# Optimization experiments

Measured on AMD Instinct MI355X. Metric: run time of the kernel, lower is better.

The kernel has to match this reference:

```python
import jax, jax.numpy as jnp
import numpy as np

B, T, E, D = 256, 128, 256, 256


def setup_inputs() -> dict:
    key = jax.random.key(0)
    ks = jax.random.split(key, 8)
    x = jax.random.normal(ks[0], (B, T, E), dtype=jnp.float32)
    # torch default Linear init: U(-1/sqrt(fan_in), 1/sqrt(fan_in)) for proj layers;
    # TreeLSTMCell.reset_parameters uses U(-1/sqrt(hidden), 1/sqrt(hidden)).
    se = 1.0 / np.sqrt(E)
    sd = 1.0 / np.sqrt(D)
    Wp = jax.random.uniform(ks[1], (E, D), jnp.float32, -se, se)
    bp = jax.random.uniform(ks[2], (D,), jnp.float32, -se, se)
    Wg = jax.random.uniform(ks[3], (E, D), jnp.float32, -se, se)
    bg = jax.random.uniform(ks[4], (D,), jnp.float32, -se, se)
    Wr = jax.random.uniform(ks[5], (2 * D, 5 * D), jnp.float32, -sd, sd)
    br = jax.random.uniform(ks[6], (5 * D,), jnp.float32, -sd, sd)
    # Valid shift-reduce sequence (right-branching): S, then (S, R) x (T-1) -> length 2T-1.
    pat = np.zeros(2 * T - 1, dtype=np.int32)
    pat[2::2] = 1  # REDUCE at odd stack-growth points
    transitions = jnp.asarray(np.broadcast_to(pat[:, None], (2 * T - 1, B)).copy())
    return {"x": x, "Wp": Wp, "bp": bp, "Wg": Wg, "bg": bg,
            "Wr": Wr, "br": br, "transitions": transitions}


def reference(x, Wp, bp, Wg, bg, Wr, br, transitions):
    Bx, Tx, _ = x.shape
    Dh = Wp.shape[1]
    # leaf transformation: c = Wx+b ; h = sigmoid(gate) * tanh(c)
    c_buf = x @ Wp + bp                                   # [B, T, D]
    h_buf = jax.nn.sigmoid(x @ Wg + bg) * jnp.tanh(c_buf)  # [B, T, D]
    buffers = jnp.concatenate([h_buf, c_buf], axis=-1)    # [B, T, 2D]

    stack0 = jnp.zeros((Bx, Tx, 2 * Dh), x.dtype)
    ptr0 = jnp.zeros((Bx,), jnp.int32)          # stack pointer (next free slot)
    bptr0 = jnp.full((Bx,), Tx - 1, jnp.int32)  # buffer pop index (pops from end)
    bidx = jnp.arange(Bx)

    def step(carry, trans_t):
        stack, ptr, bptr = carry
        is_shift = trans_t == 0
        shift_val = buffers[bidx, bptr]                       # [B, 2D]
        r = stack[bidx, jnp.maximum(ptr - 1, 0)]              # right child (top)
        l = stack[bidx, jnp.maximum(ptr - 2, 0)]              # left child
        h_l, c_l = l[:, :Dh], l[:, Dh:]
        h_r, c_r = r[:, :Dh], r[:, Dh:]
        proj = jnp.concatenate([h_l, h_r], axis=-1) @ Wr + br  # [B, 5D]
        i, f_l, f_r, g, o = jnp.split(proj, 5, axis=-1)
        c = (jax.nn.sigmoid(i) * jnp.tanh(g)
             + jax.nn.sigmoid(f_l) * c_l
             + jax.nn.sigmoid(f_r) * c_r)
        h = jax.nn.sigmoid(o) * jnp.tanh(c)
        red = jnp.concatenate([h, c], axis=-1)                # [B, 2D]
        pos = jnp.where(is_shift, ptr, jnp.maximum(ptr - 2, 0))
        val = jnp.where(is_shift[:, None], shift_val, red)
        stack = stack.at[bidx, pos].set(val)
        ptr = ptr + jnp.where(is_shift, jnp.int32(1), jnp.int32(-1))
        bptr = bptr - is_shift.astype(jnp.int32)
        return (stack, ptr, bptr), None

    (stack, ptr, _), _ = jax.lax.scan(step, (stack0, ptr0, bptr0), transitions)
    final = stack[bidx, jnp.maximum(ptr - 1, 0)][:, :Dh]  # root h states [B, D]
    return final
```

## Files before the change

kernel.cpp:

```cpp
#include <hip/hip_runtime.h>


typedef unsigned int u32;
typedef short s16x8 __attribute__((ext_vector_type(8)));
typedef float f32x4 __attribute__((ext_vector_type(4)));

#define NPAIR 128
#define ZCODE 0x801F

#define MFMA16(a, b, c) __builtin_amdgcn_mfma_f32_16x16x32_bf16((a), (b), (c), 0, 0, 0)

static __device__ __forceinline__ unsigned short f2bf(float x) {
  u32 u = __builtin_bit_cast(u32, x);
  u += 0x7fffu + ((u >> 16) & 1u);
  return (unsigned short)(u >> 16);
}
static __device__ __forceinline__ float bf2f(unsigned short s) {
  u32 u = ((u32)s) << 16;
  return __builtin_bit_cast(float, u);
}
static __device__ __forceinline__ u32 packhl(float x) {
  unsigned short hi = f2bf(x);
  unsigned short lo = f2bf(x - bf2f(hi));
  return ((u32)hi << 16) | (u32)lo;
}
static __device__ __forceinline__ float unpackhl(u32 p) {
  return bf2f((unsigned short)(p >> 16)) + bf2f((unsigned short)(p & 0xffffu));
}
static __device__ __forceinline__ void unpack8(uint4 a, uint4 b, s16x8 &hi, s16x8 &lo) {
  hi[0] = (short)(a.x >> 16); lo[0] = (short)a.x;
  hi[1] = (short)(a.y >> 16); lo[1] = (short)a.y;
  hi[2] = (short)(a.z >> 16); lo[2] = (short)a.z;
  hi[3] = (short)(a.w >> 16); lo[3] = (short)a.w;
  hi[4] = (short)(b.x >> 16); lo[4] = (short)b.x;
  hi[5] = (short)(b.y >> 16); lo[5] = (short)b.y;
  hi[6] = (short)(b.z >> 16); lo[6] = (short)b.z;
  hi[7] = (short)(b.w >> 16); lo[7] = (short)b.w;
}
static __device__ __forceinline__ void split8(const float *w, s16x8 &hi, s16x8 &lo) {
#pragma unroll
  for (int i = 0; i < 8; i++) {
    unsigned short h = f2bf(w[i]);
    hi[i] = (short)h;
    lo[i] = (short)f2bf(w[i] - bf2f(h));
  }
}
static __device__ __forceinline__ float sigm(float x) { return 1.0f / (1.0f + expf(-x)); }

__global__ __launch_bounds__(256) void pack_kernel(
    const float *__restrict__ Wp, const float *__restrict__ Wg,
    const float *__restrict__ Wr, u32 *__restrict__ Wpg_t,
    u32 *__restrict__ Wr_t, u32 *__restrict__ vstkH, float *__restrict__ vstkC) {
  int tid = blockIdx.x * 256 + threadIdx.x;
  if (tid < 512 * 256) {
    int col = tid >> 8, k = tid & 255;
    float v = (col < 256) ? Wp[k * 256 + col] : Wg[k * 256 + (col - 256)];
    Wpg_t[tid] = packhl(v);
  }
  if (tid < 1280 * 512) {
    int col = tid >> 9, k = tid & 511;
    Wr_t[tid] = packhl(Wr[k * 1280 + col]);
  }
  if (tid < 65536) {
    vstkH[31 * 65536 + tid] = 0u;
    vstkC[31 * 65536 + tid] = 0.0f;
  }
}

__global__ __launch_bounds__(256) void plan_kernel(
    const int *__restrict__ trans, int *__restrict__ planL,
    int *__restrict__ planR, int *__restrict__ planW, int *__restrict__ fdesc) {
  int b = threadIdx.x;
  int tag[16], ver[16];
#pragma unroll
  for (int i = 0; i < 16; ++i) { tag[i] = ZCODE; ver[i] = 0; }
  int ptr = 0, bptr = 127;

  auto dostep = [&](int tr, int &l, int &r, int &w) {
    if (tr == 0) {
      int pos = min(ptr, 15);
      tag[pos] = bptr & 127;
      ptr++; bptr--;
    } else {
      int pl = min(max(ptr - 2, 0), 15);
      int pr = min(max(ptr - 1, 0), 15);
      l = tag[pl];
      r = tag[pr];
      ver[pl] ^= 1;
      tag[pl] = 0x8000 | (ver[pl] << 4) | pl;
      w = pl * 2 + ver[pl];
      ptr--;
    }
  };

  for (int f = 0; f < NPAIR; ++f) {
    int l = ZCODE, r = ZCODE, w = -1;
    dostep(trans[(2 * f) * 256 + b], l, r, w);
    if (2 * f + 1 < 255) dostep(trans[(2 * f + 1) * 256 + b], l, r, w);
    planL[f * 256 + b] = l;
    planR[f * 256 + b] = r;
    planW[f * 256 + b] = w;
  }
  fdesc[b] = tag[min(max(ptr - 1, 0), 15)];
}

__global__ __launch_bounds__(64) void front_kernel(
    const float *__restrict__ x, const u32 *__restrict__ Wpg,
    const float *__restrict__ bp, const float *__restrict__ bg,
    u32 *__restrict__ h_buf, float *__restrict__ c_buf) {
  const int lane = threadIdx.x;
  const int rbase = blockIdx.x * 32;
  const int y = blockIdx.y;
  const int rlo = lane & 15;
  const int khi = (lane >> 4) * 8;

  f32x4 z = {0.f, 0.f, 0.f, 0.f};
  f32x4 aP0[8], aP1[8], aG0[8], aG1[8];
#pragma unroll
  for (int i = 0; i < 8; i++) { aP0[i] = z; aP1[i] = z; aG0[i] = z; aG1[i] = z; }

#pragma unroll 2
  for (int kt = 0; kt < 8; ++kt) {
    int k = kt * 32 + khi;
    s16x8 A0h, A0l, A1h, A1l;
    {
      const float *ap = x + (rbase + rlo) * 256 + k;
      float4 v0 = *(const float4 *)ap;
      float4 v1 = *(const float4 *)(ap + 4);
      float w[8] = {v0.x, v0.y, v0.z, v0.w, v1.x, v1.y, v1.z, v1.w};
      split8(w, A0h, A0l);
    }
    {
      const float *ap = x + (rbase + 16 + rlo) * 256 + k;
      float4 v0 = *(const float4 *)ap;
      float4 v1 = *(const float4 *)(ap + 4);
      float w[8] = {v0.x, v0.y, v0.z, v0.w, v1.x, v1.y, v1.z, v1.w};
      split8(w, A1h, A1l);
    }
#pragma unroll
    for (int nt = 0; nt < 8; ++nt) {
      int colP = y * 128 + nt * 16 + rlo;
      {
        const u32 *wp = Wpg + colP * 256 + k;
        uint4 q0 = *(const uint4 *)wp;
        uint4 q1 = *(const uint4 *)(wp + 4);
        s16x8 Bh, Bl;
        unpack8(q0, q1, Bh, Bl);
        aP0[nt] = MFMA16(A0h, Bh, aP0[nt]);
        aP0[nt] = MFMA16(A0h, Bl, aP0[nt]);
        aP0[nt] = MFMA16(A0l, Bh, aP0[nt]);
        aP1[nt] = MFMA16(A1h, Bh, aP1[nt]);
        aP1[nt] = MFMA16(A1h, Bl, aP1[nt]);
        aP1[nt] = MFMA16(A1l, Bh, aP1[nt]);
      }
      {
        const u32 *wg = Wpg + (256 + colP) * 256 + k;
        uint4 q0 = *(const uint4 *)wg;
        uint4 q1 = *(const uint4 *)(wg + 4);
        s16x8 Bh, Bl;
        unpack8(q0, q1, Bh, Bl);
        aG0[nt] = MFMA16(A0h, Bh, aG0[nt]);
        aG0[nt] = MFMA16(A0h, Bl, aG0[nt]);
        aG0[nt] = MFMA16(A0l, Bh, aG0[nt]);
        aG1[nt] = MFMA16(A1h, Bh, aG1[nt]);
        aG1[nt] = MFMA16(A1h, Bl, aG1[nt]);
        aG1[nt] = MFMA16(A1l, Bh, aG1[nt]);
      }
    }
  }
#pragma unroll
  for (int nt = 0; nt < 8; ++nt) {
    int d = y * 128 + nt * 16 + rlo;
    float bpd = bp[d], bgd = bg[d];
#pragma unroll
    for (int ri = 0; ri < 4; ++ri) {
      int r0 = rbase + (lane >> 4) * 4 + ri;
      float cv0 = aP0[nt][ri] + bpd;
      float gv0 = aG0[nt][ri] + bgd;
      c_buf[r0 * 256 + d] = cv0;
      h_buf[r0 * 256 + d] = packhl(sigm(gv0) * tanhf(cv0));
      int r1 = rbase + 16 + (lane >> 4) * 4 + ri;
      float cv1 = aP1[nt][ri] + bpd;
      float gv1 = aG1[nt][ri] + bgd;
      c_buf[r1 * 256 + d] = cv1;
      h_buf[r1 * 256 + d] = packhl(sigm(gv1) * tanhf(cv1));
    }
  }
}

__global__ __launch_bounds__(64) void step_kernel(
    const float *__restrict__ br, const u32 *__restrict__ Wr_t,
    const u32 *__restrict__ h_buf, const float *__restrict__ c_buf,
    u32 *__restrict__ vstkH, float *__restrict__ vstkC,
    const int *__restrict__ pL, const int *__restrict__ pR,
    const int *__restrict__ pW) {
  const int c = blockIdx.x;
  const int g = blockIdx.y;
  const int lane = threadIdx.x;
  const int b0 = g * 16;
  const int row = lane & 15;
  const int b = b0 + row;

  const int lcode = pL[b];
  const int rcode = pR[b];
  const int wrw = pW[b];
  if (__ballot(wrw >= 0) == 0ull) return;

  const u32 *srcL = (lcode & 0x8000)
      ? vstkH + ((((lcode & 15) * 2 + ((lcode >> 4) & 1)) * 256 + b) << 8)
      : h_buf + (((b << 7) + (lcode & 127)) << 8);
  const u32 *srcR = (rcode & 0x8000)
      ? vstkH + ((((rcode & 15) * 2 + ((rcode >> 4) & 1)) * 256 + b) << 8)
      : h_buf + (((b << 7) + (rcode & 127)) << 8);
  const int khi = (lane >> 4) * 8;

  int cl = lane & 15;
  int v2 = 32 + cl;
  int gcol0 = ((cl >> 3) * 256) + c * 8 + (cl & 7);
  int gcol1 = (((16 + cl) >> 3) * 256) + c * 8 + (cl & 7);
  int gcol2 = (v2 < 40) ? ((v2 >> 3) * 256) + c * 8 + (v2 & 7) : 0;

  f32x4 acc0 = {0.f, 0.f, 0.f, 0.f}, acc1 = acc0, acc2 = acc0;
#pragma unroll 4
  for (int kt = 0; kt < 16; ++kt) {
    int kk = kt * 32 + khi;
    const u32 *s = (kk < 256) ? (srcL + kk) : (srcR + (kk - 256));
    uint4 a0 = *(const uint4 *)s;
    uint4 a1 = *(const uint4 *)(s + 4);
    s16x8 Ah, Al;
    unpack8(a0, a1, Ah, Al);
    {
      const u32 *wp = Wr_t + gcol0 * 512 + kk;
      uint4 q0 = *(const uint4 *)wp, q1 = *(const uint4 *)(wp + 4);
      s16x8 Bh, Bl;
      unpack8(q0, q1, Bh, Bl);
      acc0 = MFMA16(Ah, Bh, acc0);
      acc0 = MFMA16(Ah, Bl, acc0);
      acc0 = MFMA16(Al, Bh, acc0);
    }
    {
      const u32 *wp = Wr_t + gcol1 * 512 + kk;
      uint4 q0 = *(const uint4 *)wp, q1 = *(const uint4 *)(wp + 4);
      s16x8 Bh, Bl;
      unpack8(q0, q1, Bh, Bl);
      acc1 = MFMA16(Ah, Bh, acc1);
      acc1 = MFMA16(Ah, Bl, acc1);
      acc1 = MFMA16(Al, Bh, acc1);
    }
    {
      const u32 *wp = Wr_t + gcol2 * 512 + kk;
      uint4 q0 = *(const uint4 *)wp, q1 = *(const uint4 *)(wp + 4);
      s16x8 Bh, Bl;
      unpack8(q0, q1, Bh, Bl);
      acc2 = MFMA16(Ah, Bh, acc2);
      acc2 = MFMA16(Ah, Bl, acc2);
      acc2 = MFMA16(Al, Bh, acc2);
    }
  }

  f32x4 flv, gv;
#pragma unroll
  for (int ri = 0; ri < 4; ++ri) {
    flv[ri] = __shfl_xor(acc0[ri], 8);
    gv[ri] = __shfl_xor(acc1[ri], 8);
  }
  int lcs[4], rcs[4], wcs[4];
#pragma unroll
  for (int ri = 0; ri < 4; ++ri) {
    int rr = (lane >> 4) * 4 + ri;
    lcs[ri] = __shfl(lcode, rr);
    rcs[ri] = __shfl(rcode, rr);
    wcs[ri] = __shfl(wrw, rr);
  }
  int colj = lane & 15;
  if (colj < 8) {
    int d = c * 8 + colj;
    float brI = br[d], brFl = br[256 + d], brFr = br[512 + d];
    float brG = br[768 + d], brO = br[1024 + d];
#pragma unroll
    for (int ri = 0; ri < 4; ++ri) {
      if (wcs[ri] >= 0) {
        int rr = (lane >> 4) * 4 + ri;
        int b2 = b0 + rr;
        int lc = lcs[ri], rc = rcs[ri];
        float c_l = (lc & 0x8000)
            ? vstkC[(((lc & 15) * 2 + ((lc >> 4) & 1)) * 256 + b2) * 256 + d]
            : c_buf[(b2 * 128 + (lc & 127)) * 256 + d];
        float c_r = (rc & 0x8000)
            ? vstkC[(((rc & 15) * 2 + ((rc >> 4) & 1)) * 256 + b2) * 256 + d]
            : c_buf[(b2 * 128 + (rc & 127)) * 256 + d];
        float ii = acc0[ri] + brI;
        float fl = flv[ri] + brFl;
        float fr = acc1[ri] + brFr;
        float gg = gv[ri] + brG;
        float oo = acc2[ri] + brO;
        float cv = sigm(ii) * tanhf(gg) + sigm(fl) * c_l + sigm(fr) * c_r;
        float hv = sigm(oo) * tanhf(cv);
        int sidx = wcs[ri];
        vstkH[(sidx * 256 + b2) * 256 + d] = packhl(hv);
        vstkC[(sidx * 256 + b2) * 256 + d] = cv;
      }
    }
  }
}

__global__ __launch_bounds__(256) void out_kernel(
    const int *__restrict__ fdesc, const u32 *__restrict__ h_buf,
    const u32 *__restrict__ vstkH, float *__restrict__ out) {
  int tid = blockIdx.x * 256 + threadIdx.x;
  int b = tid >> 8, d = tid & 255;
  int code = fdesc[b];
  u32 hv = (code & 0x8000)
      ? vstkH[(((code & 15) * 2 + ((code >> 4) & 1)) * 256 + b) * 256 + d]
      : h_buf[(b * 128 + (code & 127)) * 256 + d];
  out[tid] = unpackhl(hv);
}

extern "C" void kernel_launch(void *const *d_in, const int *in_sizes, int n_in,
                              void *d_out, int out_size, void *d_ws, size_t ws_size,
                              hipStream_t stream) {
  const float *x = (const float *)d_in[0];
  const float *Wp = (const float *)d_in[1];
  const float *bp = (const float *)d_in[2];
  const float *Wg = (const float *)d_in[3];
  const float *bg = (const float *)d_in[4];
  const float *Wr = (const float *)d_in[5];
  const float *br = (const float *)d_in[6];
  const int *trans = (const int *)d_in[7];
  float *out = (float *)d_out;

  char *ws = (char *)d_ws;
  u32 *Wr_t = (u32 *)(ws);
  u32 *Wpg = (u32 *)(ws + 2621440);
  u32 *h_buf = (u32 *)(ws + 3145728);
  float *c_buf = (float *)(ws + 36700160);
  u32 *vstkH = (u32 *)(ws + 70254592);
  float *vstkC = (float *)(ws + 78643200);
  int *planL = (int *)(ws + 87031808);
  int *planR = (int *)(ws + 87162880);
  int *planW = (int *)(ws + 87293952);
  int *fdesc = (int *)(ws + 87425024);

  pack_kernel<<<2560, 256, 0, stream>>>(Wp, Wg, Wr, Wpg, Wr_t, vstkH, vstkC);
  plan_kernel<<<1, 256, 0, stream>>>(trans, planL, planR, planW, fdesc);
  front_kernel<<<dim3(1024, 2), 64, 0, stream>>>(x, Wpg, bp, bg, h_buf, c_buf);
  for (int f = 0; f < NPAIR; ++f)
    step_kernel<<<dim3(32, 16), 64, 0, stream>>>(
        br, Wr_t, h_buf, c_buf, vstkH, vstkC,
        planL + f * 256, planR + f * 256, planW + f * 256);
  out_kernel<<<256, 256, 0, stream>>>(fdesc, h_buf, vstkH, out);
}
```

Baseline: 1.976 ms.

## Precompute buffer-leaf reduce projections in batched chunks off the sequential step path

Adds a ppre_kernel that, in chunks of steps, computes the Wr projection contributions (plus bias) from children that come from the leaf buffer. Each sequential step then only multiplies the children that live on the stack and skips the k-half for buffer operands. Also pre-packs x into hi/lo bf16 in the pack kernel, coalesces the weight-pack reads, and packs the plan tags into registers. This depends on the workspace being large enough, and the extra chunk kernels plus ppre memory traffic are interleaved into the stream.

```diff
diff --git a/kernel.cpp b/kernel.cpp
--- a/kernel.cpp
+++ b/kernel.cpp
@@ -4,9 +4,6 @@
 typedef unsigned int u32;
 typedef short s16x8 __attribute__((ext_vector_type(8)));
 typedef float f32x4 __attribute__((ext_vector_type(4)));
-
-#define NPAIR 128
-#define ZCODE 0x801F
 
 #define MFMA16(a, b, c) __builtin_amdgcn_mfma_f32_16x16x32_bf16((a), (b), (c), 0, 0, 0)
 
@@ -46,125 +43,139 @@
   }
 }
 static __device__ __forceinline__ float sigm(float x) { return 1.0f / (1.0f + expf(-x)); }
+static __device__ __forceinline__ int vslot(int code) {
+  return (code & 15) * 2 + ((code >> 4) & 1);
+}
 
 __global__ __launch_bounds__(256) void pack_kernel(
     const float *__restrict__ Wp, const float *__restrict__ Wg,
-    const float *__restrict__ Wr, u32 *__restrict__ Wpg_t,
-    u32 *__restrict__ Wr_t, u32 *__restrict__ vstkH, float *__restrict__ vstkC) {
+    const float *__restrict__ Wr, const float *__restrict__ x,
+    u32 *__restrict__ Wpg_t, u32 *__restrict__ Wr_t, u32 *__restrict__ xpk,
+    u32 *__restrict__ vstkH, float *__restrict__ vstkC, int do_x) {
   int tid = blockIdx.x * 256 + threadIdx.x;
-  if (tid < 512 * 256) {
-    int col = tid >> 8, k = tid & 255;
-    float v = (col < 256) ? Wp[k * 256 + col] : Wg[k * 256 + (col - 256)];
-    Wpg_t[tid] = packhl(v);
-  }
-  if (tid < 1280 * 512) {
-    int col = tid >> 9, k = tid & 511;
-    Wr_t[tid] = packhl(Wr[k * 1280 + col]);
+  if (tid < 131072) {
+    int isg = tid >= 65536;
+    int s = tid & 65535;
+    int k = s >> 8, col = s & 255;
+    float v = isg ? Wg[s] : Wp[s];
+    Wpg_t[(isg ? 256 + col : col) * 256 + k] = packhl(v);
+  }
+  if (tid < 655360) {
+    int k = tid / 1280;
+    int col = tid - k * 1280;
+    Wr_t[col * 512 + k] = packhl(Wr[tid]);
   }
   if (tid < 65536) {
     vstkH[31 * 65536 + tid] = 0u;
     vstkC[31 * 65536 + tid] = 0.0f;
   }
+  if (do_x && tid < 8388608) xpk[tid] = packhl(x[tid]);
 }
 
 __global__ __launch_bounds__(256) void plan_kernel(
-    const int *__restrict__ trans, int *__restrict__ planL,
-    int *__restrict__ planR, int *__restrict__ planW, int *__restrict__ fdesc) {
+    const int *__restrict__ trans, int *__restrict__ pL, int *__restrict__ pR,
+    int *__restrict__ pW, int *__restrict__ fdesc) {
   int b = threadIdx.x;
-  int tag[16], ver[16];
-#pragma unroll
-  for (int i = 0; i < 16; ++i) { tag[i] = ZCODE; ver[i] = 0; }
+  u32 t0 = 0x9F9F9F9Fu, t1 = t0, t2 = t0, t3 = t0;
+  u32 verb = 0;
   int ptr = 0, bptr = 127;
 
+  auto get = [&](int p) -> u32 {
+    u32 w = p < 8 ? (p < 4 ? t0 : t1) : (p < 12 ? t2 : t3);
+    return (w >> ((p & 3) * 8)) & 0xffu;
+  };
+  auto set = [&](int p, u32 e) {
+    u32 sh = (u32)(p & 3) * 8u;
+    u32 m = ~(0xffu << sh);
+    u32 nv = e << sh;
+    int ws = p >> 2;
+    t0 = ws == 0 ? (t0 & m) | nv : t0;
+    t1 = ws == 1 ? (t1 & m) | nv : t1;
+    t2 = ws == 2 ? (t2 & m) | nv : t2;
+    t3 = ws == 3 ? (t3 & m) | nv : t3;
+  };
   auto dostep = [&](int tr, int &l, int &r, int &w) {
     if (tr == 0) {
       int pos = min(ptr, 15);
-      tag[pos] = bptr & 127;
+      set(pos, (u32)(bptr & 127));
       ptr++; bptr--;
     } else {
       int pl = min(max(ptr - 2, 0), 15);
       int pr = min(max(ptr - 1, 0), 15);
-      l = tag[pl];
-      r = tag[pr];
-      ver[pl] ^= 1;
-      tag[pl] = 0x8000 | (ver[pl] << 4) | pl;
-      w = pl * 2 + ver[pl];
+      l = (int)get(pl);
+      r = (int)get(pr);
+      u32 v = ((verb >> pl) & 1u) ^ 1u;
+      verb = (verb & ~(1u << pl)) | (v << pl);
+      set(pl, 0x80u | (v << 4) | (u32)pl);
+      w = pl * 2 + (int)v;
       ptr--;
     }
   };
-
-  for (int f = 0; f < NPAIR; ++f) {
-    int l = ZCODE, r = ZCODE, w = -1;
+  auto ext = [&](int e) -> int { return (e & 0x80) ? (0x8000 | (e & 0x1f)) : e; };
+
+  for (int f = 0; f < 128; ++f) {
+    int l = 0x9F, r = 0x9F, w = -1;
     dostep(trans[(2 * f) * 256 + b], l, r, w);
     if (2 * f + 1 < 255) dostep(trans[(2 * f + 1) * 256 + b], l, r, w);
-    planL[f * 256 + b] = l;
-    planR[f * 256 + b] = r;
-    planW[f * 256 + b] = w;
-  }
-  fdesc[b] = tag[min(max(ptr - 1, 0), 15)];
-}
-
+    pL[f * 256 + b] = ext(l);
+    pR[f * 256 + b] = ext(r);
+    pW[f * 256 + b] = w;
+  }
+  fdesc[b] = ext((int)get(min(max(ptr - 1, 0), 15)));
+}
+
+template <int UX>
 __global__ __launch_bounds__(64) void front_kernel(
-    const float *__restrict__ x, const u32 *__restrict__ Wpg,
-    const float *__restrict__ bp, const float *__restrict__ bg,
-    u32 *__restrict__ h_buf, float *__restrict__ c_buf) {
+    const float *__restrict__ x, const u32 *__restrict__ xpk,
+    const u32 *__restrict__ Wpg, const float *__restrict__ bp,
+    const float *__restrict__ bg, u32 *__restrict__ h_buf,
+    float *__restrict__ c_buf) {
   const int lane = threadIdx.x;
-  const int rbase = blockIdx.x * 32;
+  const int rbase = blockIdx.x * 16;
   const int y = blockIdx.y;
   const int rlo = lane & 15;
   const int khi = (lane >> 4) * 8;
 
   f32x4 z = {0.f, 0.f, 0.f, 0.f};
-  f32x4 aP0[8], aP1[8], aG0[8], aG1[8];
-#pragma unroll
-  for (int i = 0; i < 8; i++) { aP0[i] = z; aP1[i] = z; aG0[i] = z; aG1[i] = z; }
+  f32x4 aP[8], aG[8];
+#pragma unroll
+  for (int i = 0; i < 8; i++) { aP[i] = z; aG[i] = z; }
 
 #pragma unroll 2
   for (int kt = 0; kt < 8; ++kt) {
     int k = kt * 32 + khi;
-    s16x8 A0h, A0l, A1h, A1l;
-    {
+    s16x8 Ah, Al;
+    if (UX) {
+      const u32 *ap = xpk + (rbase + rlo) * 256 + k;
+      uint4 a0 = *(const uint4 *)ap, a1 = *(const uint4 *)(ap + 4);
+      unpack8(a0, a1, Ah, Al);
+    } else {
       const float *ap = x + (rbase + rlo) * 256 + k;
       float4 v0 = *(const float4 *)ap;
       float4 v1 = *(const float4 *)(ap + 4);
       float w[8] = {v0.x, v0.y, v0.z, v0.w, v1.x, v1.y, v1.z, v1.w};
-      split8(w, A0h, A0l);
-    }
-    {
-      const float *ap = x + (rbase + 16 + rlo) * 256 + k;
-      float4 v0 = *(const float4 *)ap;
-      float4 v1 = *(const float4 *)(ap + 4);
-      float w[8] = {v0.x, v0.y, v0.z, v0.w, v1.x, v1.y, v1.z, v1.w};
-      split8(w, A1h, A1l);
+      split8(w, Ah, Al);
     }
 #pragma unroll
     for (int nt = 0; nt < 8; ++nt) {
       int colP = y * 128 + nt * 16 + rlo;
       {
         const u32 *wp = Wpg + colP * 256 + k;
-        uint4 q0 = *(const uint4 *)wp;
-        uint4 q1 = *(const uint4 *)(wp + 4);
+        uint4 q0 = *(const uint4 *)wp, q1 = *(const uint4 *)(wp + 4);
         s16x8 Bh, Bl;
         unpack8(q0, q1, Bh, Bl);
-        aP0[nt] = MFMA16(A0h, Bh, aP0[nt]);
-        aP0[nt] = MFMA16(A0h, Bl, aP0[nt]);
-        aP0[nt] = MFMA16(A0l, Bh, aP0[nt]);
-        aP1[nt] = MFMA16(A1h, Bh, aP1[nt]);
-        aP1[nt] = MFMA16(A1h, Bl, aP1[nt]);
-        aP1[nt] = MFMA16(A1l, Bh, aP1[nt]);
+        aP[nt] = MFMA16(Ah, Bh, aP[nt]);
+        aP[nt] = MFMA16(Ah, Bl, aP[nt]);
+        aP[nt] = MFMA16(Al, Bh, aP[nt]);
       }
       {
         const u32 *wg = Wpg + (256 + colP) * 256 + k;
-        uint4 q0 = *(const uint4 *)wg;
-        uint4 q1 = *(const uint4 *)(wg + 4);
+        uint4 q0 = *(const uint4 *)wg, q1 = *(const uint4 *)(wg + 4);
         s16x8 Bh, Bl;
         unpack8(q0, q1, Bh, Bl);
-        aG0[nt] = MFMA16(A0h, Bh, aG0[nt]);
-        aG0[nt] = MFMA16(A0h, Bl, aG0[nt]);
-        aG0[nt] = MFMA16(A0l, Bh, aG0[nt]);
-        aG1[nt] = MFMA16(A1h, Bh, aG1[nt]);
-        aG1[nt] = MFMA16(A1h, Bl, aG1[nt]);
-        aG1[nt] = MFMA16(A1l, Bh, aG1[nt]);
+        aG[nt] = MFMA16(Ah, Bh, aG[nt]);
+        aG[nt] = MFMA16(Ah, Bl, aG[nt]);
+        aG[nt] = MFMA16(Al, Bh, aG[nt]);
       }
     }
   }
@@ -174,88 +185,158 @@
     float bpd = bp[d], bgd = bg[d];
 #pragma unroll
     for (int ri = 0; ri < 4; ++ri) {
-      int r0 = rbase + (lane >> 4) * 4 + ri;
-      float cv0 = aP0[nt][ri] + bpd;
-      float gv0 = aG0[nt][ri] + bgd;
-      c_buf[r0 * 256 + d] = cv0;
-      h_buf[r0 * 256 + d] = packhl(sigm(gv0) * tanhf(cv0));
-      int r1 = rbase + 16 + (lane >> 4) * 4 + ri;
-      float cv1 = aP1[nt][ri] + bpd;
-      float gv1 = aG1[nt][ri] + bgd;
-      c_buf[r1 * 256 + d] = cv1;
-      h_buf[r1 * 256 + d] = packhl(sigm(gv1) * tanhf(cv1));
-    }
-  }
-}
-
+      int r = rbase + (lane >> 4) * 4 + ri;
+      float cv = aP[nt][ri] + bpd;
+      float gv = aG[nt][ri] + bgd;
+      c_buf[r * 256 + d] = cv;
+      h_buf[r * 256 + d] = packhl(sigm(gv) * tanhf(cv));
+    }
+  }
+}
+
+#define KSTEP_BODY(SRC, KOFF)                                                \
+  {                                                                          \
+    const u32 *s = (SRC) + kt * 32 + khi;                                    \
+    uint4 a0 = *(const uint4 *)s, a1 = *(const uint4 *)(s + 4);              \
+    s16x8 Ah, Al;                                                            \
+    unpack8(a0, a1, Ah, Al);                                                 \
+    int kk = (KOFF) + kt * 32 + khi;                                         \
+    {                                                                        \
+      const u32 *wp = Wr_t + gcol0 * 512 + kk;                               \
+      uint4 q0 = *(const uint4 *)wp, q1 = *(const uint4 *)(wp + 4);          \
+      s16x8 Bh, Bl;                                                          \
+      unpack8(q0, q1, Bh, Bl);                                               \
+      acc0 = MFMA16(Ah, Bh, acc0);                                           \
+      acc0 = MFMA16(Ah, Bl, acc0);                                           \
+      acc0 = MFMA16(Al, Bh, acc0);                                           \
+    }                                                                        \
+    {                                                                        \
+      const u32 *wp = Wr_t + gcol1 * 512 + kk;                               \
+      uint4 q0 = *(const uint4 *)wp, q1 = *(const uint4 *)(wp + 4);          \
+      s16x8 Bh, Bl;                                                          \
+      unpack8(q0, q1, Bh, Bl);                                               \
+      acc1 = MFMA16(Ah, Bh, acc1);                                           \
+      acc1 = MFMA16(Ah, Bl, acc1);                                           \
+      acc1 = MFMA16(Al, Bh, acc1);                                           \
+    }                                                                        \
+    {                                                                        \
+      const u32 *wp = Wr_t + gcol2 * 512 + kk;                               \
+      uint4 q0 = *(const uint4 *)wp, q1 = *(const uint4 *)(wp + 4);          \
+      s16x8 Bh, Bl;                                                          \
+      unpack8(q0, q1, Bh, Bl);                                               \
+      acc2 = MFMA16(Ah, Bh, acc2);                                           \
+      acc2 = MFMA16(Ah, Bl, acc2);                                           \
+      acc2 = MFMA16(Al, Bh, acc2);                                           \
+    }                                                                        \
+  }
+
+__global__ __launch_bounds__(64) void ppre_kernel(
+    const float *__restrict__ br, const u32 *__restrict__ Wr_t,
+    const u32 *__restrict__ h_buf, const u32 *__restrict__ vzero,
+    const int *__restrict__ pL, const int *__restrict__ pR,
+    const int *__restrict__ pW, float *__restrict__ ppre) {
+  const int c = blockIdx.x;
+  const int fl = blockIdx.y >> 4;
+  const int g = blockIdx.y & 15;
+  const int lane = threadIdx.x;
+  const int b0 = g * 16;
+  const int b = b0 + (lane & 15);
+
+  const int lc = pL[fl * 256 + b];
+  const int rc = pR[fl * 256 + b];
+  const int w = pW[fl * 256 + b];
+  if (__ballot(w >= 0) == 0ull) return;
+
+  const bool lbuf = (lc & 0x8000) == 0;
+  const bool rbuf = (rc & 0x8000) == 0;
+  const u32 *srcT = lbuf ? h_buf + (((b << 7) + (lc & 127)) << 8) : vzero + (b << 8);
+  const u32 *srcB = rbuf ? h_buf + (((b << 7) + (rc & 127)) << 8) : vzero + (b << 8);
+  const bool doT = __ballot(w >= 0 && lbuf) != 0ull;
+  const bool doB = __ballot(w >= 0 && rbuf) != 0ull;
+
+  const int khi = (lane >> 4) * 8;
+  const int cl = lane & 15;
+  const int v2c = 32 + cl;
+  const int gcol0 = (cl >> 3) * 256 + c * 8 + (cl & 7);
+  const int gcol1 = ((16 + cl) >> 3) * 256 + c * 8 + (cl & 7);
+  const int gcol2 = (v2c < 40) ? (v2c >> 3) * 256 + c * 8 + (v2c & 7) : 0;
+
+  f32x4 acc0 = {0.f, 0.f, 0.f, 0.f}, acc1 = acc0, acc2 = acc0;
+  if (doT) {
+#pragma unroll 4
+    for (int kt = 0; kt < 8; ++kt) KSTEP_BODY(srcT, 0)
+  }
+  if (doB) {
+#pragma unroll 4
+    for (int kt = 0; kt < 8; ++kt) KSTEP_BODY(srcB, 256)
+  }
+
+  int wcs[4];
+#pragma unroll
+  for (int ri = 0; ri < 4; ++ri) wcs[ri] = __shfl(w, (lane >> 4) * 4 + ri);
+  float br0 = br[gcol0], br1 = br[gcol1], br2 = br[gcol2];
+  float *pr = ppre + (size_t)fl * 327680;
+#pragma unroll
+  for (int ri = 0; ri < 4; ++ri) {
+    if (wcs[ri] >= 0) {
+      int b2 = b0 + (lane >> 4) * 4 + ri;
+      float *row = pr + b2 * 1280;
+      row[gcol0] = acc0[ri] + br0;
+      row[gcol1] = acc1[ri] + br1;
+      if (v2c < 40) row[gcol2] = acc2[ri] + br2;
+    }
+  }
+}
+
+template <int PPRE>
 __global__ __launch_bounds__(64) void step_kernel(
     const float *__restrict__ br, const u32 *__restrict__ Wr_t,
     const u32 *__restrict__ h_buf, const float *__restrict__ c_buf,
     u32 *__restrict__ vstkH, float *__restrict__ vstkC,
-    const int *__restrict__ pL, const int *__restrict__ pR,
-    const int *__restrict__ pW) {
+    const u32 *__restrict__ vzero, const int *__restrict__ pL,
+    const int *__restrict__ pR, const int *__restrict__ pW,
+    const float *__restrict__ ppre) {
   const int c = blockIdx.x;
   const int g = blockIdx.y;
   const int lane = threadIdx.x;
   const int b0 = g * 16;
-  const int row = lane & 15;
-  const int b = b0 + row;
-
-  const int lcode = pL[b];
-  const int rcode = pR[b];
-  const int wrw = pW[b];
-  if (__ballot(wrw >= 0) == 0ull) return;
-
-  const u32 *srcL = (lcode & 0x8000)
-      ? vstkH + ((((lcode & 15) * 2 + ((lcode >> 4) & 1)) * 256 + b) << 8)
-      : h_buf + (((b << 7) + (lcode & 127)) << 8);
-  const u32 *srcR = (rcode & 0x8000)
-      ? vstkH + ((((rcode & 15) * 2 + ((rcode >> 4) & 1)) * 256 + b) << 8)
-      : h_buf + (((b << 7) + (rcode & 127)) << 8);
+  const int b = b0 + (lane & 15);
+
+  const int lc = pL[b];
+  const int rc = pR[b];
+  const int w = pW[b];
+  if (__ballot(w >= 0) == 0ull) return;
+
+  const bool lval = (lc & 0x8000) != 0;
+  const bool rval = (rc & 0x8000) != 0;
+  const u32 *srcT, *srcB;
+  if (PPRE) {
+    srcT = lval ? vstkH + ((vslot(lc) * 256 + b) << 8) : vzero + (b << 8);
+    srcB = rval ? vstkH + ((vslot(rc) * 256 + b) << 8) : vzero + (b << 8);
+  } else {
+    srcT = lval ? vstkH + ((vslot(lc) * 256 + b) << 8)
+                : h_buf + (((b << 7) + (lc & 127)) << 8);
+    srcB = rval ? vstkH + ((vslot(rc) * 256 + b) << 8)
+                : h_buf + (((b << 7) + (rc & 127)) << 8);
+  }
+  const bool doT = PPRE ? (__ballot(w >= 0 && lval) != 0ull) : true;
+  const bool doB = PPRE ? (__ballot(w >= 0 && rval) != 0ull) : true;
+
   const int khi = (lane >> 4) * 8;
-
-  int cl = lane & 15;
-  int v2 = 32 + cl;
-  int gcol0 = ((cl >> 3) * 256) + c * 8 + (cl & 7);
-  int gcol1 = (((16 + cl) >> 3) * 256) + c * 8 + (cl & 7);
-  int gcol2 = (v2 < 40) ? ((v2 >> 3) * 256) + c * 8 + (v2 & 7) : 0;
+  const int cl = lane & 15;
+  const int v2c = 32 + cl;
+  const int gcol0 = (cl >> 3) * 256 + c * 8 + (cl & 7);
+  const int gcol1 = ((16 + cl) >> 3) * 256 + c * 8 + (cl & 7);
+  const int gcol2 = (v2c < 40) ? (v2c >> 3) * 256 + c * 8 + (v2c & 7) : 0;
 
   f32x4 acc0 = {0.f, 0.f, 0.f, 0.f}, acc1 = acc0, acc2 = acc0;
+  if (doT) {
 #pragma unroll 4
-  for (int kt = 0; kt < 16; ++kt) {
-    int kk = kt * 32 + khi;
-    const u32 *s = (kk < 256) ? (srcL + kk) : (srcR + (kk - 256));
-    uint4 a0 = *(const uint4 *)s;
-    uint4 a1 = *(const uint4 *)(s + 4);
-    s16x8 Ah, Al;
-    unpack8(a0, a1, Ah, Al);
-    {
-      const u32 *wp = Wr_t + gcol0 * 512 + kk;
-      uint4 q0 = *(const uint4 *)wp, q1 = *(const uint4 *)(wp + 4);
-      s16x8 Bh, Bl;
-      unpack8(q0, q1, Bh, Bl);
-      acc0 = MFMA16(Ah, Bh, acc0);
-      acc0 = MFMA16(Ah, Bl, acc0);
-      acc0 = MFMA16(Al, Bh, acc0);
-    }
-    {
-      const u32 *wp = Wr_t + gcol1 * 512 + kk;
-      uint4 q0 = *(const uint4 *)wp, q1 = *(const uint4 *)(wp + 4);
-      s16x8 Bh, Bl;
-      unpack8(q0, q1, Bh, Bl);
-      acc1 = MFMA16(Ah, Bh, acc1);
-      acc1 = MFMA16(Ah, Bl, acc1);
-      acc1 = MFMA16(Al, Bh, acc1);
-    }
-    {
-      const u32 *wp = Wr_t + gcol2 * 512 + kk;
-      uint4 q0 = *(const uint4 *)wp, q1 = *(const uint4 *)(wp + 4);
-      s16x8 Bh, Bl;
-      unpack8(q0, q1, Bh, Bl);
-      acc2 = MFMA16(Ah, Bh, acc2);
-      acc2 = MFMA16(Ah, Bl, acc2);
-      acc2 = MFMA16(Al, Bh, acc2);
-    }
+    for (int kt = 0; kt < 8; ++kt) KSTEP_BODY(srcT, 0)
+  }
+  if (doB) {
+#pragma unroll 4
+    for (int kt = 0; kt < 8; ++kt) KSTEP_BODY(srcB, 256)
   }
 
   f32x4 flv, gv;
@@ -268,32 +349,42 @@
 #pragma unroll
   for (int ri = 0; ri < 4; ++ri) {
     int rr = (lane >> 4) * 4 + ri;
-    lcs[ri] = __shfl(lcode, rr);
-    rcs[ri] = __shfl(rcode, rr);
-    wcs[ri] = __shfl(wrw, rr);
+    lcs[ri] = __shfl(lc, rr);
+    rcs[ri] = __shfl(rc, rr);
+    wcs[ri] = __shfl(w, rr);
   }
   int colj = lane & 15;
   if (colj < 8) {
     int d = c * 8 + colj;
-    float brI = br[d], brFl = br[256 + d], brFr = br[512 + d];
-    float brG = br[768 + d], brO = br[1024 + d];
+    float brI = 0, brFl = 0, brFr = 0, brG = 0, brO = 0;
+    if (!PPRE) {
+      brI = br[d]; brFl = br[256 + d]; brFr = br[512 + d];
+      brG = br[768 + d]; brO = br[1024 + d];
+    }
 #pragma unroll
     for (int ri = 0; ri < 4; ++ri) {
       if (wcs[ri] >= 0) {
-        int rr = (lane >> 4) * 4 + ri;
-        int b2 = b0 + rr;
-        int lc = lcs[ri], rc = rcs[ri];
-        float c_l = (lc & 0x8000)
-            ? vstkC[(((lc & 15) * 2 + ((lc >> 4) & 1)) * 256 + b2) * 256 + d]
-            : c_buf[(b2 * 128 + (lc & 127)) * 256 + d];
-        float c_r = (rc & 0x8000)
-            ? vstkC[(((rc & 15) * 2 + ((rc >> 4) & 1)) * 256 + b2) * 256 + d]
-            : c_buf[(b2 * 128 + (rc & 127)) * 256 + d];
-        float ii = acc0[ri] + brI;
-        float fl = flv[ri] + brFl;
-        float fr = acc1[ri] + brFr;
-        float gg = gv[ri] + brG;
-        float oo = acc2[ri] + brO;
+        int b2 = b0 + (lane >> 4) * 4 + ri;
+        int lc2 = lcs[ri], rc2 = rcs[ri];
+        float c_l = (lc2 & 0x8000)
+                        ? vstkC[(vslot(lc2) * 256 + b2) * 256 + d]
+                        : c_buf[(b2 * 128 + (lc2 & 127)) * 256 + d];
+        float c_r = (rc2 & 0x8000)
+                        ? vstkC[(vslot(rc2) * 256 + b2) * 256 + d]
+                        : c_buf[(b2 * 128 + (rc2 & 127)) * 256 + d];
+        float pI, pFl, pFr, pG, pO;
+        if (PPRE) {
+          const float *row = ppre + (size_t)b2 * 1280;
+          pI = row[d]; pFl = row[256 + d]; pFr = row[512 + d];
+          pG = row[768 + d]; pO = row[1024 + d];
+        } else {
+          pI = brI; pFl = brFl; pFr = brFr; pG = brG; pO = brO;
+        }
+        float ii = acc0[ri] + pI;
+        float fl = flv[ri] + pFl;
+        float fr = acc1[ri] + pFr;
+        float gg = gv[ri] + pG;
+        float oo = acc2[ri] + pO;
         float cv = sigm(ii) * tanhf(gg) + sigm(fl) * c_l + sigm(fr) * c_r;
         float hv = sigm(oo) * tanhf(cv);
         int sidx = wcs[ri];
@@ -311,8 +402,8 @@
   int b = tid >> 8, d = tid & 255;
   int code = fdesc[b];
   u32 hv = (code & 0x8000)
-      ? vstkH[(((code & 15) * 2 + ((code >> 4) & 1)) * 256 + b) * 256 + d]
-      : h_buf[(b * 128 + (code & 127)) * 256 + d];
+               ? vstkH[(vslot(code) * 256 + b) * 256 + d]
+               : h_buf[(b * 128 + (code & 127)) * 256 + d];
   out[tid] = unpackhl(hv);
 }
 
@@ -340,13 +431,59 @@
   int *planR = (int *)(ws + 87162880);
   int *planW = (int *)(ws + 87293952);
   int *fdesc = (int *)(ws + 87425024);
-
-  pack_kernel<<<2560, 256, 0, stream>>>(Wp, Wg, Wr, Wpg, Wr_t, vstkH, vstkC);
+  const u32 *vzero = vstkH + 31 * 65536;
+
+  const size_t fixed_end = 87426048;
+  const size_t slotB = 1310720;
+  const size_t xpkB = 33554432;
+  size_t avail = ws_size > fixed_end ? ws_size - fixed_end : 0;
+  size_t tail = fixed_end;
+  int use_xpk = 0;
+  if (avail >= xpkB + 4 * slotB) { use_xpk = 1; tail += xpkB; avail -= xpkB; }
+  u32 *xpk = (u32 *)(ws + fixed_end);
+  int R = (int)(avail / slotB);
+  if (R > 32) R = 32;
+  R &= ~1;
+  int use_ppre = (R >= 2);
+  int C = use_ppre ? R / 2 : 0;
+  float *ppre = (float *)(ws + tail);
+
+  pack_kernel<<<use_xpk ? 32768 : 2560, 256, 0, stream>>>(
+      Wp, Wg, Wr, x, Wpg, Wr_t, xpk, vstkH, vstkC, use_xpk);
   plan_kernel<<<1, 256, 0, stream>>>(trans, planL, planR, planW, fdesc);
-  front_kernel<<<dim3(1024, 2), 64, 0, stream>>>(x, Wpg, bp, bg, h_buf, c_buf);
-  for (int f = 0; f < NPAIR; ++f)
-    step_kernel<<<dim3(32, 16), 64, 0, stream>>>(
-        br, Wr_t, h_buf, c_buf, vstkH, vstkC,
-        planL + f * 256, planR + f * 256, planW + f * 256);
+  if (use_xpk)
+    front_kernel<1><<<dim3(2048, 2), 64, 0, stream>>>(x, xpk, Wpg, bp, bg, h_buf, c_buf);
+  else
+    front_kernel<0><<<dim3(2048, 2), 64, 0, stream>>>(x, xpk, Wpg, bp, bg, h_buf, c_buf);
+
+  if (use_ppre) {
+    int nch = (128 + C - 1) / C;
+    auto pre = [&](int k) {
+      int f0 = k * C;
+      int Ck = min(C, 128 - f0);
+      ppre_kernel<<<dim3(32, Ck * 16), 64, 0, stream>>>(
+          br, Wr_t, h_buf, vzero, planL + f0 * 256, planR + f0 * 256,
+          planW + f0 * 256, ppre + (size_t)((k & 1) * C) * 327680);
+    };
+    pre(0);
+    if (nch > 1) pre(1);
+    for (int k = 0; k < nch; ++k) {
+      int f0 = k * C;
+      int Ck = min(C, 128 - f0);
+      for (int fl = 0; fl < Ck; ++fl) {
+        int f = f0 + fl;
+        step_kernel<1><<<dim3(32, 16), 64, 0, stream>>>(
+            br, Wr_t, h_buf, c_buf, vstkH, vstkC, vzero, planL + f * 256,
+            planR + f * 256, planW + f * 256,
+            ppre + (size_t)((k & 1) * C + fl) * 327680);
+      }
+      if (k + 2 < nch) pre(k + 2);
+    }
+  } else {
+    for (int f = 0; f < 128; ++f)
+      step_kernel<0><<<dim3(32, 16), 64, 0, stream>>>(
+          br, Wr_t, h_buf, c_buf, vstkH, vstkC, vzero, planL + f * 256,
+          planR + f * 256, planW + f * 256, nullptr);
+  }
   out_kernel<<<256, 256, 0, stream>>>(fdesc, h_buf, vstkH, out);
 }
```

Result: slower. 2.249 ms (+13.8%).
